# Performance work log

Measured on AMD Instinct MI355X. Metric: run time of the kernel, lower is better.

## Reference

```python
import jax, jax.numpy as jnp
import numpy as np

B, T, F = 32, 4096, 512
H = 512

def setup_inputs() -> dict:
    key = jax.random.key(0)
    k1, k2, k3, k4, k5 = jax.random.split(key, 5)
    enc = jax.random.normal(k1, (B, T, F), dtype=jnp.float32)
    dec = jax.random.normal(k2, (B, F), dtype=jnp.float32)
    # Dense kernels (no bias), scaled like Glorot-ish init
    W1 = jax.random.normal(k3, (F, H), dtype=jnp.float32) / np.sqrt(F)
    W2 = jax.random.normal(k4, (F, H), dtype=jnp.float32) / np.sqrt(F)
    V = jax.random.normal(k5, (H, 1), dtype=jnp.float32) / np.sqrt(H)
    return {"encoder_outputs": enc, "dec_output": dec, "W1": W1, "W2": W2, "V": V}

def reference(encoder_outputs, dec_output, W1, W2, V):
    # Bahdanau additive attention, fully vectorized over time_steps
    # (the original runs this step-by-step via K.rnn; state is unchanged,
    # so the computation is embarrassingly parallel over t).
    w1_e = jnp.einsum('btf,fh->bth', encoder_outputs, W1)   # [B,T,H]
    w2_d = jnp.einsum('bf,fh->bh', dec_output, W2)          # [B,H]
    scores = jnp.einsum('bth,h->bt', jnp.tanh(w1_e + w2_d[:, None, :]), V[:, 0])  # [B,T]
    return jax.nn.softmax(scores, axis=1)
```

## Files before the change

kernel.cpp:

```cpp
#include <hip/hip_runtime.h>
#include <hip/hip_bf16.h>

#define B_ 32
#define T_ 4096
#define F_ 512
#define H_ 512

typedef float floatx4 __attribute__((ext_vector_type(4)));
typedef short short8 __attribute__((ext_vector_type(8)));

__device__ __forceinline__ unsigned pack2_bf16(float a, float b) {
  unsigned ua = __float_as_uint(a);
  unsigned ub = __float_as_uint(b);
  ua = (ua + 0x7FFFu + ((ua >> 16) & 1u)) >> 16;
  ub = (ub + 0x7FFFu + ((ub >> 16) & 1u)) & 0xFFFF0000u;
  return ua | ub;
}

__device__ __forceinline__ unsigned short f2bf16(float a) {
  unsigned ua = __float_as_uint(a);
  return (unsigned short)((ua + 0x7FFFu + ((ua >> 16) & 1u)) >> 16);
}

__device__ __forceinline__ float tanh_fast(float x) {
  float e = __expf(2.0f * x);
  return 1.0f - __fdividef(2.0f, e + 1.0f);
}

__device__ __forceinline__ void async_load16(const void* g, void* l) {
  __builtin_amdgcn_global_load_lds(
      (const __attribute__((address_space(1))) void*)g,
      (__attribute__((address_space(3))) void*)l, 16, 0, 0);
}

__global__ void prep_w1t(const float* __restrict__ W1, unsigned short* __restrict__ W1T) {
  __shared__ float tile[32][33];
  const int tx = threadIdx.x, ty = threadIdx.y;
  const int f = blockIdx.y * 32 + ty;
  const int h = blockIdx.x * 32 + tx;
  tile[ty][tx] = W1[f * H_ + h];
  __syncthreads();
  const int ho = blockIdx.x * 32 + ty;
  const int fo = blockIdx.y * 32 + tx;
  W1T[ho * F_ + fo] = f2bf16(tile[tx][ty]);
}

__global__ void prep_w2d(const float* __restrict__ dec, const float* __restrict__ W2,
                         float* __restrict__ w2d) {
  const int b = blockIdx.x, h = threadIdx.x;
  float s0 = 0.f, s1 = 0.f, s2 = 0.f, s3 = 0.f;
  for (int f = 0; f < F_; f += 4) {
    s0 += dec[b * F_ + f + 0] * W2[(f + 0) * H_ + h];
    s1 += dec[b * F_ + f + 1] * W2[(f + 1) * H_ + h];
    s2 += dec[b * F_ + f + 2] * W2[(f + 2) * H_ + h];
    s3 += dec[b * F_ + f + 3] * W2[(f + 3) * H_ + h];
  }
  w2d[b * H_ + h] = (s0 + s1) + (s2 + s3);
}

__global__ __launch_bounds__(256) void fused_score(
    const float* __restrict__ enc, const unsigned short* __restrict__ W1T,
    const float* __restrict__ w2d, const float* __restrict__ V,
    float* __restrict__ scores) {
  __shared__ __align__(16) unsigned short As[128 * 32];
  __shared__ __align__(16) unsigned short Bs[128 * 32];

  const int tid = threadIdx.x;
  const int bid = blockIdx.x;
  const int m_blk = bid >> 2;
  const int n_blk = bid & 3;
  const int lane = tid & 63;
  const int wave = tid >> 6;
  const int wm = wave >> 1;
  const int wn = wave & 1;
  const int quad = lane >> 4;
  const int l16 = lane & 15;

  const int arow = tid >> 3;
  const int acol = (tid & 7) * 4;
  const float* aptr = enc + (size_t)(m_blk * 128 + arow) * F_ + acol;

  const int nb0 = wave * 32;
  const unsigned short* bsrc0 =
      W1T + (size_t)(n_blk * 128 + nb0 + (lane >> 2)) * F_ + (lane & 3) * 8;
  const unsigned short* bsrc1 = bsrc0 + 16 * F_;
  unsigned short* bdst0 = &Bs[nb0 * 32];
  unsigned short* bdst1 = &Bs[(nb0 + 16) * 32];

  floatx4 acc[4][4];
#pragma unroll
  for (int i = 0; i < 4; i++)
#pragma unroll
    for (int j = 0; j < 4; j++) acc[i][j] = (floatx4){0.f, 0.f, 0.f, 0.f};

  for (int ks = 0; ks < 16; ++ks) {
    const int k0 = ks * 32;
    __syncthreads();
    async_load16(bsrc0 + k0, bdst0);
    async_load16(bsrc1 + k0, bdst1);
#pragma unroll
    for (int rr = 0; rr < 4; ++rr) {
      const float4 v = *(const float4*)(aptr + rr * 32 * F_ + k0);
      uint2 pk;
      pk.x = pack2_bf16(v.x, v.y);
      pk.y = pack2_bf16(v.z, v.w);
      *(uint2*)&As[(arow + rr * 32) * 32 + acol] = pk;
    }
    __syncthreads();

    short8 af[4], bfr[4];
#pragma unroll
    for (int i = 0; i < 4; i++)
      af[i] = *(const short8*)&As[(wm * 64 + i * 16 + l16) * 32 + quad * 8];
#pragma unroll
    for (int j = 0; j < 4; j++)
      bfr[j] = *(const short8*)&Bs[(wn * 64 + j * 16 + l16) * 32 + quad * 8];
#pragma unroll
    for (int i = 0; i < 4; i++)
#pragma unroll
      for (int j = 0; j < 4; j++)
        acc[i][j] = __builtin_amdgcn_mfma_f32_16x16x32_bf16(af[i], bfr[j], acc[i][j], 0, 0, 0);
  }

  const int b = m_blk >> 5;
  float w2v[4], vv[4];
#pragma unroll
  for (int j = 0; j < 4; j++) {
    const int h = n_blk * 128 + wn * 64 + j * 16 + l16;
    w2v[j] = w2d[b * H_ + h];
    vv[j] = V[h];
  }
  float rs[4][4];
#pragma unroll
  for (int i = 0; i < 4; i++)
#pragma unroll
    for (int r = 0; r < 4; r++) {
      float s = 0.f;
#pragma unroll
      for (int j = 0; j < 4; j++) s += tanh_fast(acc[i][j][r] + w2v[j]) * vv[j];
      rs[i][r] = s;
    }
#pragma unroll
  for (int i = 0; i < 4; i++)
#pragma unroll
    for (int r = 0; r < 4; r++) {
      float s = rs[i][r];
      s += __shfl_xor(s, 1, 16);
      s += __shfl_xor(s, 2, 16);
      s += __shfl_xor(s, 4, 16);
      s += __shfl_xor(s, 8, 16);
      rs[i][r] = s;
    }
  if (l16 == 0) {
#pragma unroll
    for (int i = 0; i < 4; i++)
#pragma unroll
      for (int r = 0; r < 4; r++)
        atomicAdd(&scores[m_blk * 128 + wm * 64 + i * 16 + quad * 4 + r], rs[i][r]);
  }
}

__global__ __launch_bounds__(256) void softmax_rows(const float* __restrict__ scores,
                                                    float* __restrict__ out) {
  const int b = blockIdx.x;
  const int tid = threadIdx.x;
  const int wave = tid >> 6;
  __shared__ float red[4];
  float v[16];
  float mx = -1e30f;
#pragma unroll
  for (int i = 0; i < 16; i++) {
    v[i] = scores[b * T_ + i * 256 + tid];
    mx = fmaxf(mx, v[i]);
  }
#pragma unroll
  for (int o = 32; o > 0; o >>= 1) mx = fmaxf(mx, __shfl_xor(mx, o, 64));
  if ((tid & 63) == 0) red[wave] = mx;
  __syncthreads();
  mx = fmaxf(fmaxf(red[0], red[1]), fmaxf(red[2], red[3]));
  __syncthreads();
  float sum = 0.f;
#pragma unroll
  for (int i = 0; i < 16; i++) {
    v[i] = __expf(v[i] - mx);
    sum += v[i];
  }
#pragma unroll
  for (int o = 32; o > 0; o >>= 1) sum += __shfl_xor(sum, o, 64);
  if ((tid & 63) == 0) red[wave] = sum;
  __syncthreads();
  sum = (red[0] + red[1]) + (red[2] + red[3]);
  const float inv = 1.0f / sum;
#pragma unroll
  for (int i = 0; i < 16; i++) out[b * T_ + i * 256 + tid] = v[i] * inv;
}

extern "C" void kernel_launch(void* const* d_in, const int* in_sizes, int n_in,
                              void* d_out, int out_size, void* d_ws, size_t ws_size,
                              hipStream_t stream) {
  const float* enc = (const float*)d_in[0];
  const float* dec = (const float*)d_in[1];
  const float* W1 = (const float*)d_in[2];
  const float* W2 = (const float*)d_in[3];
  const float* V = (const float*)d_in[4];
  float* out = (float*)d_out;

  char* ws = (char*)d_ws;
  float* scores = (float*)ws;
  unsigned short* W1T = (unsigned short*)(ws + 524288);
  float* w2d = (float*)(ws + 1048576);

  (void)in_sizes; (void)n_in; (void)out_size; (void)ws_size;

  hipMemsetAsync(scores, 0, B_ * T_ * sizeof(float), stream);
  prep_w1t<<<dim3(16, 16), dim3(32, 32), 0, stream>>>(W1, W1T);
  prep_w2d<<<dim3(32), dim3(512), 0, stream>>>(dec, W2, w2d);
  fused_score<<<dim3(4096), dim3(256), 0, stream>>>(enc, W1T, w2d, V, scores);
  softmax_rows<<<dim3(32), dim3(256), 0, stream>>>(scores, out);
}
```

Baseline: 499.7 us.

## Double-buffer GEMM tiles with register prefetch, swizzle LDS, remap blocks per XCD

Double-buffers the A and B tiles of the fused score GEMM in LDS and prefetches the next encoder tile into registers while the MFMAs run, leaving one barrier per k-step. It pads the A tile stride and XOR-swizzles the B tile to cut LDS bank conflicts. It remaps block ids so that blocks sharing encoder rows land on the same XCD for L2 reuse, and sets an occupancy hint. It also splits prep_w2d across more blocks. The cost is more LDS and register pressure, which may limit occupancy.

```diff
diff --git a/kernel.cpp b/kernel.cpp
--- a/kernel.cpp
+++ b/kernel.cpp
@@ -45,9 +45,11 @@
   W1T[ho * F_ + fo] = f2bf16(tile[tx][ty]);
 }
 
-__global__ void prep_w2d(const float* __restrict__ dec, const float* __restrict__ W2,
-                         float* __restrict__ w2d) {
-  const int b = blockIdx.x, h = threadIdx.x;
+__global__ __launch_bounds__(128) void prep_w2d(const float* __restrict__ dec,
+                                                const float* __restrict__ W2,
+                                                float* __restrict__ w2d) {
+  const int b = blockIdx.x;
+  const int h = blockIdx.y * 128 + threadIdx.x;
   float s0 = 0.f, s1 = 0.f, s2 = 0.f, s3 = 0.f;
   for (int f = 0; f < F_; f += 4) {
     s0 += dec[b * F_ + f + 0] * W2[(f + 0) * H_ + h];
@@ -58,17 +60,19 @@
   w2d[b * H_ + h] = (s0 + s1) + (s2 + s3);
 }
 
-__global__ __launch_bounds__(256) void fused_score(
+__global__ __launch_bounds__(256, 3) void fused_score(
     const float* __restrict__ enc, const unsigned short* __restrict__ W1T,
     const float* __restrict__ w2d, const float* __restrict__ V,
     float* __restrict__ scores) {
-  __shared__ __align__(16) unsigned short As[128 * 32];
-  __shared__ __align__(16) unsigned short Bs[128 * 32];
+  __shared__ __align__(16) unsigned short As[2][128 * 40];
+  __shared__ __align__(16) unsigned short Bs[2][128 * 32];
 
   const int tid = threadIdx.x;
   const int bid = blockIdx.x;
-  const int m_blk = bid >> 2;
-  const int n_blk = bid & 3;
+  const int xcd = bid & 7;
+  const int ii = bid >> 3;
+  const int n_blk = ii & 3;
+  const int m_blk = xcd + ((ii >> 2) << 3);
   const int lane = tid & 63;
   const int wave = tid >> 6;
   const int wm = wave >> 1;
@@ -76,16 +80,16 @@
   const int quad = lane >> 4;
   const int l16 = lane & 15;
 
-  const int arow = tid >> 3;
-  const int acol = (tid & 7) * 4;
+  const int arow = tid >> 2;
+  const int acol = (tid & 3) * 8;
   const float* aptr = enc + (size_t)(m_blk * 128 + arow) * F_ + acol;
 
   const int nb0 = wave * 32;
+  const int bl_n = lane >> 2;
+  const int bl_c = (lane & 3) ^ (bl_n & 3);
   const unsigned short* bsrc0 =
-      W1T + (size_t)(n_blk * 128 + nb0 + (lane >> 2)) * F_ + (lane & 3) * 8;
+      W1T + (size_t)(n_blk * 128 + nb0 + bl_n) * F_ + bl_c * 8;
   const unsigned short* bsrc1 = bsrc0 + 16 * F_;
-  unsigned short* bdst0 = &Bs[nb0 * 32];
-  unsigned short* bdst1 = &Bs[(nb0 + 16) * 32];
 
   floatx4 acc[4][4];
 #pragma unroll
@@ -93,33 +97,67 @@
 #pragma unroll
     for (int j = 0; j < 4; j++) acc[i][j] = (floatx4){0.f, 0.f, 0.f, 0.f};
 
+  float4 a_pre[4];
+
+#pragma unroll
+  for (int rr = 0; rr < 2; ++rr) {
+    a_pre[rr * 2 + 0] = *(const float4*)(aptr + rr * 64 * F_ + 0);
+    a_pre[rr * 2 + 1] = *(const float4*)(aptr + rr * 64 * F_ + 4);
+  }
+#pragma unroll
+  for (int rr = 0; rr < 2; ++rr) {
+    uint4 pk;
+    pk.x = pack2_bf16(a_pre[rr * 2].x, a_pre[rr * 2].y);
+    pk.y = pack2_bf16(a_pre[rr * 2].z, a_pre[rr * 2].w);
+    pk.z = pack2_bf16(a_pre[rr * 2 + 1].x, a_pre[rr * 2 + 1].y);
+    pk.w = pack2_bf16(a_pre[rr * 2 + 1].z, a_pre[rr * 2 + 1].w);
+    *(uint4*)&As[0][(arow + rr * 64) * 40 + acol] = pk;
+  }
+  async_load16(bsrc0, &Bs[0][nb0 * 32]);
+  async_load16(bsrc1, &Bs[0][(nb0 + 16) * 32]);
+  __syncthreads();
+
   for (int ks = 0; ks < 16; ++ks) {
-    const int k0 = ks * 32;
-    __syncthreads();
-    async_load16(bsrc0 + k0, bdst0);
-    async_load16(bsrc1 + k0, bdst1);
-#pragma unroll
-    for (int rr = 0; rr < 4; ++rr) {
-      const float4 v = *(const float4*)(aptr + rr * 32 * F_ + k0);
-      uint2 pk;
-      pk.x = pack2_bf16(v.x, v.y);
-      pk.y = pack2_bf16(v.z, v.w);
-      *(uint2*)&As[(arow + rr * 32) * 32 + acol] = pk;
-    }
-    __syncthreads();
+    const int cur = ks & 1;
+    const int nxt = cur ^ 1;
+
+    if (ks < 15) {
+      const int k1 = (ks + 1) * 32;
+#pragma unroll
+      for (int rr = 0; rr < 2; ++rr) {
+        a_pre[rr * 2 + 0] = *(const float4*)(aptr + rr * 64 * F_ + k1);
+        a_pre[rr * 2 + 1] = *(const float4*)(aptr + rr * 64 * F_ + k1 + 4);
+      }
+      async_load16(bsrc0 + k1, &Bs[nxt][nb0 * 32]);
+      async_load16(bsrc1 + k1, &Bs[nxt][(nb0 + 16) * 32]);
+    }
 
     short8 af[4], bfr[4];
 #pragma unroll
     for (int i = 0; i < 4; i++)
-      af[i] = *(const short8*)&As[(wm * 64 + i * 16 + l16) * 32 + quad * 8];
+      af[i] = *(const short8*)&As[cur][(wm * 64 + i * 16 + l16) * 40 + quad * 8];
 #pragma unroll
     for (int j = 0; j < 4; j++)
-      bfr[j] = *(const short8*)&Bs[(wn * 64 + j * 16 + l16) * 32 + quad * 8];
+      bfr[j] = *(const short8*)&Bs[cur][(wn * 64 + j * 16 + l16) * 32 +
+                                        ((quad ^ (l16 & 3)) * 8)];
 #pragma unroll
     for (int i = 0; i < 4; i++)
 #pragma unroll
       for (int j = 0; j < 4; j++)
         acc[i][j] = __builtin_amdgcn_mfma_f32_16x16x32_bf16(af[i], bfr[j], acc[i][j], 0, 0, 0);
+
+    if (ks < 15) {
+#pragma unroll
+      for (int rr = 0; rr < 2; ++rr) {
+        uint4 pk;
+        pk.x = pack2_bf16(a_pre[rr * 2].x, a_pre[rr * 2].y);
+        pk.y = pack2_bf16(a_pre[rr * 2].z, a_pre[rr * 2].w);
+        pk.z = pack2_bf16(a_pre[rr * 2 + 1].x, a_pre[rr * 2 + 1].y);
+        pk.w = pack2_bf16(a_pre[rr * 2 + 1].z, a_pre[rr * 2 + 1].w);
+        *(uint4*)&As[nxt][(arow + rr * 64) * 40 + acol] = pk;
+      }
+    }
+    __syncthreads();
   }
 
   const int b = m_blk >> 5;
@@ -214,7 +252,7 @@
 
   hipMemsetAsync(scores, 0, B_ * T_ * sizeof(float), stream);
   prep_w1t<<<dim3(16, 16), dim3(32, 32), 0, stream>>>(W1, W1T);
-  prep_w2d<<<dim3(32), dim3(512), 0, stream>>>(dec, W2, w2d);
+  prep_w2d<<<dim3(32, 4), dim3(128), 0, stream>>>(dec, W2, w2d);
   fused_score<<<dim3(4096), dim3(256), 0, stream>>>(enc, W1T, w2d, V, scores);
   softmax_rows<<<dim3(32), dim3(256), 0, stream>>>(scores, out);
 }
```

Result: faster. 477.9 us (-4.4%).
